# Kernel tuning notes

Measured on AMD Instinct MI355X. Metric: run time of the kernel, lower is better.

## Reference

```python
import jax, jax.numpy as jnp
import numpy as np

H = 1024  # hidden_dim; GRU hidden size is H+1, embedding_dim = 2*H


def _bigru_scan(h0, Wih_f, Whh_f, bih_f, bhh_f, Wih_b, Whh_b, bih_b, bhh_b):
    """h0: (T, 2, H+1). Runs the per-token recurrence of AnswerSynthesisEncoder.

    At each step the torch code feeds the previous step's output y (2H+2,) back
    in as the GRU *input* x = y[:2H].reshape(2,H).sum(0), and uses the token
    embedding (+f_s,f_e) reshaped to (2, H+1) as the initial hidden state h_0
    of the bidirectional, seq_len=1 GRU. Since h_0 does not depend on the
    carry, the hidden-side gate preactivations are precomputed as one GEMM.
    """
    Hh = H + 1
    gh_f = h0[:, 0] @ Whh_f.T + bhh_f  # (T, 3*(H+1))
    gh_b = h0[:, 1] @ Whh_b.T + bhh_b

    def cell(x, h, gh, Wih, bih):
        gi = Wih @ x + bih
        i_r, i_z, i_n = jnp.split(gi, 3)
        h_r, h_z, h_n = jnp.split(gh, 3)
        r = jax.nn.sigmoid(i_r + h_r)
        z = jax.nn.sigmoid(i_z + h_z)
        n = jnp.tanh(i_n + r * h_n)
        return (1.0 - z) * n + z * h

    def step(y, inp):
        h0_t, ghf_t, ghb_t = inp
        x = y[: 2 * H].reshape(2, H).sum(axis=0)  # (H,)
        yf = cell(x, h0_t[0], ghf_t, Wih_f, bih_f)
        yb = cell(x, h0_t[1], ghb_t, Wih_b, bih_b)
        y_new = jnp.concatenate([yf, yb])  # (2H+2,)
        return y_new, y_new

    y0 = jnp.zeros(2 * Hh, dtype=h0.dtype)
    _, outs = jax.lax.scan(step, y0, (h0, gh_f, gh_b))  # (T, 2H+2)
    # final slice: reshape(2, H+1)[:, :H] per token -> concat of both halves' first H
    return jnp.concatenate([outs[:, :H], outs[:, Hh : Hh + H]], axis=1)  # (T, 2H)


def setup_inputs() -> dict:
    key = jax.random.key(0)
    ks = jax.random.split(key, 12)
    Hh = H + 1
    s = 0.02
    return {
        "e_q": jax.random.normal(ks[0], (512, 2 * H), jnp.float32),
        "e_p": jax.random.normal(ks[1], (4096, 2 * H), jnp.float32),
        "f_s": jax.random.uniform(ks[2], (4096, 1), jnp.float32),
        "f_e": jax.random.uniform(ks[3], (4096, 1), jnp.float32),
        "Wih_f": jax.random.normal(ks[4], (3 * Hh, H), jnp.float32) * s,
        "Whh_f": jax.random.normal(ks[5], (3 * Hh, Hh), jnp.float32) * s,
        "bih_f": jax.random.normal(ks[6], (3 * Hh,), jnp.float32) * s,
        "bhh_f": jax.random.normal(ks[7], (3 * Hh,), jnp.float32) * s,
        "Wih_b": jax.random.normal(ks[8], (3 * Hh, H), jnp.float32) * s,
        "Whh_b": jax.random.normal(ks[9], (3 * Hh, Hh), jnp.float32) * s,
        "bih_b": jax.random.normal(ks[10], (3 * Hh,), jnp.float32) * s,
        "bhh_b": jax.random.normal(ks[11], (3 * Hh,), jnp.float32) * s,
    }


def reference(e_q, e_p, f_s, f_e, Wih_f, Whh_f, bih_f, bhh_f, Wih_b, Whh_b, bih_b, bhh_b):
    Hh = H + 1
    # h_0 per passage token: cat([e_p_t, f_s_t, f_e_t]).reshape(2, H+1)
    h0_p = jnp.concatenate([e_p, f_s, f_e], axis=1).reshape(-1, 2, Hh)
    # h_0 per query token: cat([e_q_t, 0, 0]).reshape(2, H+1)
    zq = jnp.zeros((e_q.shape[0], 2), e_q.dtype)
    h0_q = jnp.concatenate([e_q, zq], axis=1).reshape(-1, 2, Hh)
    h_p = _bigru_scan(h0_p, Wih_f, Whh_f, bih_f, bhh_f, Wih_b, Whh_b, bih_b, bhh_b)
    h_q = _bigru_scan(h0_q, Wih_f, Whh_f, bih_f, bhh_f, Wih_b, Whh_b, bih_b, bhh_b)
    return (h_q, h_p)
```

## Files before the change

kernel.cpp:

```cpp
#include <hip/hip_runtime.h>
#include <stdint.h>


#define H   1024
#define HH  1025
#define N3  3075
#define TQ  512
#define TP  4096
#define MTOT 4608
#define GTOT 2050
#define GH_ELEMS (MTOT * N3)

typedef unsigned long long ull;

__device__ __forceinline__ float sigm(float x) { return 1.f / (1.f + __expf(-x)); }
__device__ __forceinline__ float fast_tanh(float x) {
    float e = __expf(2.f * x);
    return (e - 1.f) / (e + 1.f);
}

__global__ __launch_bounds__(256, 2) void gh_gemm(
    const float* __restrict__ eq, const float* __restrict__ ep,
    const float* __restrict__ fs, const float* __restrict__ fe,
    const float* __restrict__ Whh_f, const float* __restrict__ bhh_f,
    const float* __restrict__ Whh_b, const float* __restrict__ bhh_b,
    float* __restrict__ ghf, float* __restrict__ ghb)
{
    const int dir = blockIdx.z;
    const float* W  = dir ? Whh_b : Whh_f;
    const float* bh = dir ? bhh_b : bhh_f;
    float* gh = dir ? ghb : ghf;
    const int n0 = blockIdx.x * 128;
    const int m0 = blockIdx.y * 128;

    __shared__ float As[16][132];
    __shared__ float Bs[16][132];

    float acc[8][8];
#pragma unroll
    for (int i = 0; i < 8; i++)
#pragma unroll
        for (int j = 0; j < 8; j++) acc[i][j] = 0.f;

    const int tid = threadIdx.x;
    const int tx = tid & 15, ty = tid >> 4;

    for (int k0 = 0; k0 < HH; k0 += 16) {
#pragma unroll
        for (int u = 0; u < 8; u++) {
            int lin = tid + 256 * u;
            int k = lin & 15;
            int m = lin >> 4;
            int gm = m0 + m;
            int gk = k0 + k;
            float v = 0.f;
            if (gk < HH) {
                bool isq = gm < TQ;
                const float* e = isq ? eq : ep;
                int t = isq ? gm : gm - TQ;
                if (dir == 0)            v = e[(size_t)t * 2048 + gk];
                else if (gk < 1023)      v = e[(size_t)t * 2048 + 1025 + gk];
                else if (!isq)           v = (gk == 1023) ? fs[t] : fe[t];
            }
            As[k][m] = v;
        }
#pragma unroll
        for (int u = 0; u < 8; u++) {
            int lin = tid + 256 * u;
            int k = lin & 15;
            int r = lin >> 4;
            int gr = n0 + r, gk = k0 + k;
            Bs[k][r] = (gr < N3 && gk < HH) ? W[(size_t)gr * HH + gk] : 0.f;
        }
        __syncthreads();
#pragma unroll
        for (int kk = 0; kk < 16; kk++) {
            float4 a0 = *(const float4*)&As[kk][ty * 4];
            float4 a1 = *(const float4*)&As[kk][64 + ty * 4];
            float4 b0 = *(const float4*)&Bs[kk][tx * 4];
            float4 b1 = *(const float4*)&Bs[kk][64 + tx * 4];
            float a[8] = {a0.x, a0.y, a0.z, a0.w, a1.x, a1.y, a1.z, a1.w};
            float b[8] = {b0.x, b0.y, b0.z, b0.w, b1.x, b1.y, b1.z, b1.w};
#pragma unroll
            for (int i = 0; i < 8; i++)
#pragma unroll
                for (int j = 0; j < 8; j++) acc[i][j] += a[i] * b[j];
        }
        __syncthreads();
    }
#pragma unroll
    for (int i = 0; i < 8; i++) {
        int gm = m0 + ((i < 4) ? (ty * 4 + i) : (64 + ty * 4 + i - 4));
#pragma unroll
        for (int j = 0; j < 8; j++) {
            int gr = n0 + ((j < 4) ? (tx * 4 + j) : (64 + tx * 4 + j - 4));
            if (gr < N3) gh[(size_t)gm * N3 + gr] = acc[i][j] + bh[gr];
        }
    }
}

__global__ __launch_bounds__(256, 1) void bigru_scan(
    const float* __restrict__ eq, const float* __restrict__ ep,
    const float* __restrict__ fs, const float* __restrict__ fe,
    const float* __restrict__ Wih_f, const float* __restrict__ bih_f,
    const float* __restrict__ Wih_b, const float* __restrict__ bih_b,
    const float* __restrict__ ghf, const float* __restrict__ ghb,
    ull* __restrict__ comm,
    float* __restrict__ out)
{
    __shared__ float xsh[2][2][1024];

    const int tid  = threadIdx.x;
    const int wave = tid >> 6;
    const int lane = tid & 63;
    const int gbase = blockIdx.x * 12 + wave * 3;

    float wreg[9][16];
    float breg[9];
    int   dre[3], je[3];
    bool  vale[3];
#pragma unroll
    for (int e = 0; e < 3; e++) {
        int g = gbase + e;
        bool v = (g < GTOT);
        int gc = v ? g : 0;
        int dir = gc / HH;
        int j = gc % HH;
        dre[e] = dir; je[e] = j; vale[e] = v;
        const float* Wih = dir ? Wih_b : Wih_f;
        const float* bih = dir ? bih_b : bih_f;
#pragma unroll
        for (int gate = 0; gate < 3; gate++) {
            const float* wr = Wih + (size_t)(gate * HH + j) * H;
#pragma unroll
            for (int i = 0; i < 4; i++) {
                float4 w4 = *(const float4*)(wr + i * 256 + lane * 4);
                wreg[e * 3 + gate][i * 4 + 0] = w4.x;
                wreg[e * 3 + gate][i * 4 + 1] = w4.y;
                wreg[e * 3 + gate][i * 4 + 2] = w4.z;
                wreg[e * 3 + gate][i * 4 + 3] = w4.w;
            }
            breg[e * 3 + gate] = bih[gate * HH + j];
        }
    }

    int sgh[3], sh0[3], sspec[3];
#pragma unroll
    for (int e = 0; e < 3; e++) {
        sgh[e]   = __builtin_amdgcn_readfirstlane(dre[e] * GH_ELEMS + je[e]);
        sh0[e]   = __builtin_amdgcn_readfirstlane(dre[e] ? (1025 + je[e]) : je[e]);
        sspec[e] = __builtin_amdgcn_readfirstlane(
                       (dre[e] && je[e] >= 1023) ? (je[e] - 1022) : 0);
    }
    const float* ghAll = ghf;

    float ghcP[9], h0cP[3], ghcQ[9], h0cQ[3];

    auto loadP = [&](int tt, float gh9[9], float h03[3]) {
        size_t base = (size_t)(TQ + tt) * N3;
#pragma unroll
        for (int e = 0; e < 3; e++) {
#pragma unroll
            for (int gate = 0; gate < 3; gate++)
                gh9[e * 3 + gate] = ghAll[base + (size_t)sgh[e] + gate * HH];
            h03[e] = (sspec[e] == 0) ? ep[(size_t)tt * 2048 + sh0[e]]
                   : (sspec[e] == 1) ? fs[tt] : fe[tt];
        }
    };
    auto loadQ = [&](int tt, float gh9[9], float h03[3]) {
        size_t base = (size_t)tt * N3;
#pragma unroll
        for (int e = 0; e < 3; e++) {
#pragma unroll
            for (int gate = 0; gate < 3; gate++)
                gh9[e * 3 + gate] = ghAll[base + (size_t)sgh[e] + gate * HH];
            h03[e] = (sspec[e] == 0) ? eq[(size_t)tt * 2048 + sh0[e]] : 0.f;
        }
    };

    loadP(0, ghcP, h0cP);
    loadQ(0, ghcQ, h0cQ);

    ull* commP = comm;
    ull* commQ = comm + 2 * GTOT;

    for (int t = 0; t < TP; t++) {
        const bool doq = (t < TQ);
        const int par = t & 1;

        if (t == 0) {
#pragma unroll
            for (int u = 0; u < 4; u++) {
                int j = tid + 256 * u;
                xsh[par][0][j] = 0.f;
                xsh[par][1][j] = 0.f;
            }
        } else {
            const int slot = (t + 1) & 1;
            const unsigned tag = (unsigned)t;
            ull* cp = commP + slot * GTOT;
            ull* cq = commQ + slot * GTOT;
            int idx[8];
#pragma unroll
            for (int u = 0; u < 4; u++) {
                int j = tid + 256 * u;
                idx[2 * u]     = j;
                idx[2 * u + 1] = (j == 0) ? 1024 : (1025 + j - 1);
            }
            ull vp[8], vq[8];
#pragma unroll
            for (int u = 0; u < 8; u++)
                vp[u] = __hip_atomic_load(&cp[idx[u]], __ATOMIC_RELAXED, __HIP_MEMORY_SCOPE_AGENT);
            if (doq) {
#pragma unroll
                for (int u = 0; u < 8; u++)
                    vq[u] = __hip_atomic_load(&cq[idx[u]], __ATOMIC_RELAXED, __HIP_MEMORY_SCOPE_AGENT);
            }
            bool done = false;
            while (!done) {
                done = true;
#pragma unroll
                for (int u = 0; u < 8; u++) {
                    if ((unsigned)(vp[u] >> 32) != tag) {
                        done = false;
                        vp[u] = __hip_atomic_load(&cp[idx[u]], __ATOMIC_RELAXED, __HIP_MEMORY_SCOPE_AGENT);
                    }
                }
                if (doq) {
#pragma unroll
                    for (int u = 0; u < 8; u++) {
                        if ((unsigned)(vq[u] >> 32) != tag) {
                            done = false;
                            vq[u] = __hip_atomic_load(&cq[idx[u]], __ATOMIC_RELAXED, __HIP_MEMORY_SCOPE_AGENT);
                        }
                    }
                }
            }
#pragma unroll
            for (int u = 0; u < 4; u++) {
                int j = tid + 256 * u;
                xsh[par][0][j] = __uint_as_float((unsigned)vp[2 * u]) +
                                 __uint_as_float((unsigned)vp[2 * u + 1]);
            }
            if (doq) {
#pragma unroll
                for (int u = 0; u < 4; u++) {
                    int j = tid + 256 * u;
                    xsh[par][1][j] = __uint_as_float((unsigned)vq[2 * u]) +
                                     __uint_as_float((unsigned)vq[2 * u + 1]);
                }
            }
        }
        __syncthreads();

        float ghnP[9], h0nP[3], ghnQ[9], h0nQ[3];
        const bool ldn = (t + 1) < TP;
        const bool ldq = (t + 1) < TQ;
        if (ldn) loadP(t + 1, ghnP, h0nP);
        if (ldq) loadQ(t + 1, ghnQ, h0nQ);

        float accp[9];
        {
            float x[16];
#pragma unroll
            for (int i = 0; i < 4; i++) {
                float4 x4 = *(const float4*)&xsh[par][0][i * 256 + lane * 4];
                x[i * 4 + 0] = x4.x; x[i * 4 + 1] = x4.y;
                x[i * 4 + 2] = x4.z; x[i * 4 + 3] = x4.w;
            }
#pragma unroll
            for (int r = 0; r < 9; r++) {
                float s = 0.f;
#pragma unroll
                for (int i = 0; i < 16; i++) s += wreg[r][i] * x[i];
                accp[r] = s;
            }
        }
#pragma unroll
        for (int r = 0; r < 9; r++) {
            float v = accp[r];
#pragma unroll
            for (int off = 32; off > 0; off >>= 1) v += __shfl_xor(v, off, 64);
            accp[r] = v + breg[r];
        }

        float accq[9];
        if (doq) {
            float x[16];
#pragma unroll
            for (int i = 0; i < 4; i++) {
                float4 x4 = *(const float4*)&xsh[par][1][i * 256 + lane * 4];
                x[i * 4 + 0] = x4.x; x[i * 4 + 1] = x4.y;
                x[i * 4 + 2] = x4.z; x[i * 4 + 3] = x4.w;
            }
#pragma unroll
            for (int r = 0; r < 9; r++) {
                float s = 0.f;
#pragma unroll
                for (int i = 0; i < 16; i++) s += wreg[r][i] * x[i];
#pragma unroll
                for (int off = 32; off > 0; off >>= 1) s += __shfl_xor(s, off, 64);
                accq[r] = s + breg[r];
            }
        }

        const ull tagout = ((ull)(unsigned)(t + 1)) << 32;
        float yP[3], yQ[3];
#pragma unroll
        for (int e = 0; e < 3; e++) {
            float r = sigm(accp[e * 3 + 0] + ghcP[e * 3 + 0]);
            float z = sigm(accp[e * 3 + 1] + ghcP[e * 3 + 1]);
            float n = fast_tanh(accp[e * 3 + 2] + r * ghcP[e * 3 + 2]);
            yP[e] = (1.f - z) * n + z * h0cP[e];
            if (lane == 0 && vale[e]) {
                ull pk = tagout | (ull)__float_as_uint(yP[e]);
                __hip_atomic_store(&commP[par * GTOT + (gbase + e)], pk,
                                   __ATOMIC_RELAXED, __HIP_MEMORY_SCOPE_AGENT);
            }
        }
        if (doq) {
#pragma unroll
            for (int e = 0; e < 3; e++) {
                float r = sigm(accq[e * 3 + 0] + ghcQ[e * 3 + 0]);
                float z = sigm(accq[e * 3 + 1] + ghcQ[e * 3 + 1]);
                float n = fast_tanh(accq[e * 3 + 2] + r * ghcQ[e * 3 + 2]);
                yQ[e] = (1.f - z) * n + z * h0cQ[e];
                if (lane == 0 && vale[e]) {
                    ull pk = tagout | (ull)__float_as_uint(yQ[e]);
                    __hip_atomic_store(&commQ[par * GTOT + (gbase + e)], pk,
                                       __ATOMIC_RELAXED, __HIP_MEMORY_SCOPE_AGENT);
                }
            }
        }
        if (lane == 0) {
#pragma unroll
            for (int e = 0; e < 3; e++) {
                if (vale[e] && je[e] < H) {
                    out[(size_t)TQ * 2048 + (size_t)t * 2048 + dre[e] * H + je[e]] = yP[e];
                    if (doq)
                        out[(size_t)t * 2048 + dre[e] * H + je[e]] = yQ[e];
                }
            }
        }

        if (ldn) {
#pragma unroll
            for (int i = 0; i < 9; i++) ghcP[i] = ghnP[i];
#pragma unroll
            for (int e = 0; e < 3; e++) h0cP[e] = h0nP[e];
        }
        if (ldq) {
#pragma unroll
            for (int i = 0; i < 9; i++) ghcQ[i] = ghnQ[i];
#pragma unroll
            for (int e = 0; e < 3; e++) h0cQ[e] = h0nQ[e];
        }
    }
}

extern "C" void kernel_launch(void* const* d_in, const int* in_sizes, int n_in,
                              void* d_out, int out_size, void* d_ws, size_t ws_size,
                              hipStream_t stream) {
    const float* eq    = (const float*)d_in[0];
    const float* ep    = (const float*)d_in[1];
    const float* fs    = (const float*)d_in[2];
    const float* fe    = (const float*)d_in[3];
    const float* Wih_f = (const float*)d_in[4];
    const float* Whh_f = (const float*)d_in[5];
    const float* bih_f = (const float*)d_in[6];
    const float* bhh_f = (const float*)d_in[7];
    const float* Wih_b = (const float*)d_in[8];
    const float* Whh_b = (const float*)d_in[9];
    const float* bih_b = (const float*)d_in[10];
    const float* bhh_b = (const float*)d_in[11];
    float* out = (float*)d_out;

    const size_t ghElems = (size_t)GH_ELEMS;
    float* ghf = (float*)d_ws;
    float* ghb = ghf + ghElems;
    size_t commOff = ((2 * ghElems * sizeof(float)) + 4095) & ~(size_t)4095;
    ull* comm = (ull*)((char*)d_ws + commOff);

    hipMemsetAsync(comm, 0, (size_t)4 * GTOT * sizeof(ull), stream);

    dim3 ggrid((N3 + 127) / 128, MTOT / 128, 2);
    gh_gemm<<<ggrid, 256, 0, stream>>>(eq, ep, fs, fe, Whh_f, bhh_f, Whh_b, bhh_b, ghf, ghb);

    bigru_scan<<<dim3(171), dim3(256), 0, stream>>>(
        eq, ep, fs, fe, Wih_f, bih_f, Wih_b, bih_b, ghf, ghb, comm, out);
}
```

Baseline: 14.51 ms.

## Compute hidden-gate GEMM with bf16 MFMA using split-precision activations

Replaces the FP32 SIMT tiled GEMM that precomputes hidden-side gate preactivations with a bf16 matrix-core kernel using mfma_f32_16x16x32_bf16. Activations are split into high and low bf16 parts to retain precision, while the weight matrix is rounded to a single bf16. The tile shape changes to 64x128 per block with each wave owning a 16-row strip. This targets the GEMM's arithmetic cost but adds rounding error from bf16 weights.

```diff
diff --git a/kernel.cpp b/kernel.cpp
--- a/kernel.cpp
+++ b/kernel.cpp
@@ -12,6 +12,8 @@
 #define GH_ELEMS (MTOT * N3)
 
 typedef unsigned long long ull;
+typedef __attribute__((ext_vector_type(8))) short short8;
+typedef __attribute__((ext_vector_type(4))) float f32x4;
 
 __device__ __forceinline__ float sigm(float x) { return 1.f / (1.f + __expf(-x)); }
 __device__ __forceinline__ float fast_tanh(float x) {
@@ -19,7 +21,16 @@
     return (e - 1.f) / (e + 1.f);
 }
 
-__global__ __launch_bounds__(256, 2) void gh_gemm(
+__device__ __forceinline__ unsigned short f2bf(float f) {
+    unsigned u = __float_as_uint(f);
+    unsigned r = (u + 0x7FFFu + ((u >> 16) & 1u)) >> 16;
+    return (unsigned short)r;
+}
+__device__ __forceinline__ float bf2f(unsigned short h) {
+    return __uint_as_float(((unsigned)h) << 16);
+}
+
+__global__ __launch_bounds__(256, 2) void gh_gemm_mfma(
     const float* __restrict__ eq, const float* __restrict__ ep,
     const float* __restrict__ fs, const float* __restrict__ fe,
     const float* __restrict__ Whh_f, const float* __restrict__ bhh_f,
@@ -31,28 +42,26 @@
     const float* bh = dir ? bhh_b : bhh_f;
     float* gh = dir ? ghb : ghf;
     const int n0 = blockIdx.x * 128;
-    const int m0 = blockIdx.y * 128;
-
-    __shared__ float As[16][132];
-    __shared__ float Bs[16][132];
-
-    float acc[8][8];
-#pragma unroll
-    for (int i = 0; i < 8; i++)
-#pragma unroll
-        for (int j = 0; j < 8; j++) acc[i][j] = 0.f;
-
-    const int tid = threadIdx.x;
-    const int tx = tid & 15, ty = tid >> 4;
-
-    for (int k0 = 0; k0 < HH; k0 += 16) {
+    const int m0 = blockIdx.y * 64;
+    const int tid  = threadIdx.x;
+    const int wave = tid >> 6;
+    const int lane = tid & 63;
+
+    __shared__ __align__(16) unsigned short Ah[64][40];
+    __shared__ __align__(16) unsigned short Al[64][40];
+    __shared__ __align__(16) unsigned short Bs[128][40];
+
+    f32x4 acc[8];
+#pragma unroll
+    for (int c = 0; c < 8; c++) acc[c] = (f32x4){0.f, 0.f, 0.f, 0.f};
+
+    for (int kc = 0; kc < 33; kc++) {
+        const int k0 = kc * 32;
 #pragma unroll
         for (int u = 0; u < 8; u++) {
-            int lin = tid + 256 * u;
-            int k = lin & 15;
-            int m = lin >> 4;
-            int gm = m0 + m;
-            int gk = k0 + k;
+            int lin = u * 256 + tid;
+            int row = lin >> 5, k = lin & 31;
+            int gm = m0 + row, gk = k0 + k;
             float v = 0.f;
             if (gk < HH) {
                 bool isq = gm < TQ;
@@ -62,39 +71,43 @@
                 else if (gk < 1023)      v = e[(size_t)t * 2048 + 1025 + gk];
                 else if (!isq)           v = (gk == 1023) ? fs[t] : fe[t];
             }
-            As[k][m] = v;
-        }
-#pragma unroll
-        for (int u = 0; u < 8; u++) {
-            int lin = tid + 256 * u;
-            int k = lin & 15;
-            int r = lin >> 4;
+            unsigned short h = f2bf(v);
+            Ah[row][k] = h;
+            Al[row][k] = f2bf(v - bf2f(h));
+        }
+#pragma unroll
+        for (int u = 0; u < 16; u++) {
+            int lin = u * 256 + tid;
+            int r = lin >> 5, k = lin & 31;
             int gr = n0 + r, gk = k0 + k;
-            Bs[k][r] = (gr < N3 && gk < HH) ? W[(size_t)gr * HH + gk] : 0.f;
+            float v = (gr < N3 && gk < HH) ? W[(size_t)gr * HH + gk] : 0.f;
+            Bs[r][k] = f2bf(v);
         }
         __syncthreads();
-#pragma unroll
-        for (int kk = 0; kk < 16; kk++) {
-            float4 a0 = *(const float4*)&As[kk][ty * 4];
-            float4 a1 = *(const float4*)&As[kk][64 + ty * 4];
-            float4 b0 = *(const float4*)&Bs[kk][tx * 4];
-            float4 b1 = *(const float4*)&Bs[kk][64 + tx * 4];
-            float a[8] = {a0.x, a0.y, a0.z, a0.w, a1.x, a1.y, a1.z, a1.w};
-            float b[8] = {b0.x, b0.y, b0.z, b0.w, b1.x, b1.y, b1.z, b1.w};
-#pragma unroll
-            for (int i = 0; i < 8; i++)
-#pragma unroll
-                for (int j = 0; j < 8; j++) acc[i][j] += a[i] * b[j];
+
+        const int arow = wave * 16 + (lane & 15);
+        const int koff = (lane >> 4) * 8;
+        short8 ah = *(const short8*)&Ah[arow][koff];
+        short8 al = *(const short8*)&Al[arow][koff];
+#pragma unroll
+        for (int c = 0; c < 8; c++) {
+            short8 b = *(const short8*)&Bs[c * 16 + (lane & 15)][koff];
+            acc[c] = __builtin_amdgcn_mfma_f32_16x16x32_bf16(ah, b, acc[c], 0, 0, 0);
+            acc[c] = __builtin_amdgcn_mfma_f32_16x16x32_bf16(al, b, acc[c], 0, 0, 0);
         }
         __syncthreads();
     }
-#pragma unroll
-    for (int i = 0; i < 8; i++) {
-        int gm = m0 + ((i < 4) ? (ty * 4 + i) : (64 + ty * 4 + i - 4));
-#pragma unroll
-        for (int j = 0; j < 8; j++) {
-            int gr = n0 + ((j < 4) ? (tx * 4 + j) : (64 + tx * 4 + j - 4));
-            if (gr < N3) gh[(size_t)gm * N3 + gr] = acc[i][j] + bh[gr];
+
+#pragma unroll
+    for (int c = 0; c < 8; c++) {
+        int col = n0 + c * 16 + (lane & 15);
+        if (col < N3) {
+            float bias = bh[col];
+#pragma unroll
+            for (int r = 0; r < 4; r++) {
+                int row = m0 + wave * 16 + (lane >> 4) * 4 + r;
+                gh[(size_t)row * N3 + col] = acc[c][r] + bias;
+            }
         }
     }
 }
@@ -383,8 +396,8 @@
 
     hipMemsetAsync(comm, 0, (size_t)4 * GTOT * sizeof(ull), stream);
 
-    dim3 ggrid((N3 + 127) / 128, MTOT / 128, 2);
-    gh_gemm<<<ggrid, 256, 0, stream>>>(eq, ep, fs, fe, Whh_f, bhh_f, Whh_b, bhh_b, ghf, ghb);
+    dim3 ggrid((N3 + 127) / 128, MTOT / 64, 2);
+    gh_gemm_mfma<<<ggrid, 256, 0, stream>>>(eq, ep, fs, fe, Whh_f, bhh_f, Whh_b, bhh_b, ghf, ghb);
 
     bigru_scan<<<dim3(171), dim3(256), 0, stream>>>(
         eq, ep, fs, fe, Wih_f, bih_f, Wih_b, bih_b, ghf, ghb, comm, out);
```

Result: faster. 14.20 ms (-2.1%).
